# Performance work log

Hardware: AMD Instinct MI355X
Metric: run time of the kernel (lower is better)

Reference implementation:

```python
import jax, jax.numpy as jnp
import numpy as np

N_NODES = 100000
N_EDGES = 3200000
N_GRAPHS = 512
N_LAYERS = 4
D = 24  # in/out channels of every TransformerConv (mask keeps all 24 features)


def _linear_params(key, fan_in, fan_out):
    k1, k2 = jax.random.split(key)
    bound = 1.0 / np.sqrt(fan_in)
    W = jax.random.uniform(k1, (fan_in, fan_out), minval=-bound, maxval=bound, dtype=jnp.float32)
    b = jax.random.uniform(k2, (fan_out,), minval=-bound, maxval=bound, dtype=jnp.float32)
    return W, b


def setup_inputs() -> dict:
    key = jax.random.key(0)
    ks = jax.random.split(key, 32)
    x = jax.random.normal(ks[0], (N_NODES, D), dtype=jnp.float32)
    edge_index = jax.random.randint(ks[1], (2, N_EDGES), 0, N_NODES, dtype=jnp.int64)
    batch = jnp.sort(jax.random.randint(ks[2], (N_NODES,), 0, N_GRAPHS, dtype=jnp.int64))
    gf = jax.random.normal(ks[3], (N_GRAPHS, 6), dtype=jnp.float32)

    # TransformerConv params per layer: lin_query/key/value/skip, all Linear(D, D) with bias
    Wq, bq, Wk, bk, Wv, bv, Ws, bs = [], [], [], [], [], [], [], []
    for l in range(N_LAYERS):
        kk = jax.random.split(ks[4 + l], 4)
        for W_list, b_list, kw in ((Wq, bq, kk[0]), (Wk, bk, kk[1]), (Wv, bv, kk[2]), (Ws, bs, kk[3])):
            W, b = _linear_params(kw, D, D)
            W_list.append(W); b_list.append(b)
    stack = lambda xs: jnp.stack(xs, axis=0)

    gfW1, gfb1 = _linear_params(ks[10], 6, 12)
    gfW2, gfb2 = _linear_params(ks[11], 12, 12)
    W1, b1 = _linear_params(ks[12], 36, 128)
    W2, b2 = _linear_params(ks[13], 128, 128)
    W3, b3 = _linear_params(ks[14], 128, 1)

    return dict(x=x, edge_index=edge_index, batch=batch, gf=gf,
                Wq=stack(Wq), bq=stack(bq), Wk=stack(Wk), bk=stack(bk),
                Wv=stack(Wv), bv=stack(bv), Ws=stack(Ws), bs=stack(bs),
                gfW1=gfW1, gfb1=gfb1, gfW2=gfW2, gfb2=gfb2,
                W1=W1, b1=b1, W2=W2, b2=b2, W3=W3, b3=b3)


def _transformer_conv(x, src, dst, Wq, bq, Wk, bk, Wv, bv, Ws, bs):
    # PyG TransformerConv, heads=1: alpha_e = softmax_dst((q[dst].k[src])/sqrt(D));
    # out = sum_e alpha_e * v[src] (scattered to dst) + lin_skip(x)
    n = x.shape[0]
    q = x @ Wq + bq
    k = x @ Wk + bk
    v = x @ Wv + bv
    logits = jnp.sum(q[dst] * k[src], axis=-1) * (1.0 / np.sqrt(D))  # [E]
    m = jax.ops.segment_max(logits, dst, num_segments=n)  # [N]; -inf for empty dst (unused)
    e = jnp.exp(logits - m[dst])
    denom = jax.ops.segment_sum(e, dst, num_segments=n) + 1e-16
    alpha = e / denom[dst]  # [E]
    agg = jax.ops.segment_sum(alpha[:, None] * v[src], dst, num_segments=n)  # [N, D]
    return agg + (x @ Ws + bs)


def reference(x, edge_index, batch, gf, Wq, bq, Wk, bk, Wv, bv, Ws, bs,
              gfW1, gfb1, gfW2, gfb2, W1, b1, W2, b2, W3, b3):
    src, dst = edge_index[0], edge_index[1]
    h = x  # mask keeps all 24 features
    for l in range(N_LAYERS):
        h = jax.nn.relu(_transformer_conv(h, src, dst, Wq[l], bq[l], Wk[l], bk[l],
                                          Wv[l], bv[l], Ws[l], bs[l]))
    # global_mean_pool over ragged graph batch
    sums = jax.ops.segment_sum(h, batch, num_segments=N_GRAPHS)
    counts = jax.ops.segment_sum(jnp.ones((h.shape[0],), h.dtype), batch, num_segments=N_GRAPHS)
    pooled = sums / jnp.maximum(counts, 1.0)[:, None]  # [G, 24]
    g = jax.nn.relu(gf @ gfW1 + gfb1)
    g = jax.nn.relu(g @ gfW2 + gfb2)  # [G, 12]
    z = jnp.concatenate([pooled, g], axis=1)  # [G, 36]
    z = jax.nn.relu(z @ W1 + b1)
    z = jax.nn.relu(z @ W2 + b2)
    z = z @ W3 + b3
    return jnp.squeeze(z, axis=-1)  # [G]
```

## Files before the change

### kernel.cpp

```cpp
#include <hip/hip_runtime.h>
#include <hip/hip_fp16.h>
#include <math.h>

#define N_NODES  100000
#define N_EDGES  3200000
#define N_GRAPHS 512
#define DCH      24
#define NLAYERS  4

#define BINSHIFT 9
#define BINSZ    512
#define NBINS    196
#define NBINS_P  200
#define CAP      17408
#define EPB      8000
#define NB_PART  400

#define KVROW    64

__global__ __launch_bounds__(256) void lin_kernel(
    const float* __restrict__ h,
    const float* __restrict__ Wq, const float* __restrict__ bq,
    const float* __restrict__ Wk, const float* __restrict__ bk,
    const float* __restrict__ Wv, const float* __restrict__ bv,
    const float* __restrict__ Ws, const float* __restrict__ bs,
    float* __restrict__ q, __half* __restrict__ kv, float* __restrict__ skip)
{
    __shared__ float sW[4 * 576];
    __shared__ float sb[4 * 24];
    for (int i = threadIdx.x; i < 576; i += blockDim.x) {
        sW[0 * 576 + i] = Wq[i];
        sW[1 * 576 + i] = Wk[i];
        sW[2 * 576 + i] = Wv[i];
        sW[3 * 576 + i] = Ws[i];
    }
    if (threadIdx.x < 24) {
        sb[0 * 24 + threadIdx.x] = bq[threadIdx.x];
        sb[1 * 24 + threadIdx.x] = bk[threadIdx.x];
        sb[2 * 24 + threadIdx.x] = bv[threadIdx.x];
        sb[3 * 24 + threadIdx.x] = bs[threadIdx.x];
    }
    __syncthreads();

    int node = blockIdx.x * blockDim.x + threadIdx.x;
    if (node >= N_NODES) return;

    float hx[24];
    const float4* hp = (const float4*)(h + (size_t)node * DCH);
    #pragma unroll
    for (int t = 0; t < 6; t++) {
        float4 f = hp[t];
        hx[4*t] = f.x; hx[4*t+1] = f.y; hx[4*t+2] = f.z; hx[4*t+3] = f.w;
    }

    #pragma unroll
    for (int mtx = 0; mtx < 4; mtx++) {
        float o[24];
        #pragma unroll
        for (int c = 0; c < 24; c++) o[c] = sb[mtx * 24 + c];
        #pragma unroll
        for (int ci = 0; ci < 24; ci++) {
            float hv = hx[ci];
            #pragma unroll
            for (int c = 0; c < 24; c++)
                o[c] += hv * sW[mtx * 576 + ci * 24 + c];
        }
        if (mtx == 0 || mtx == 3) {
            float* dst = (mtx == 0) ? (q + (size_t)node * DCH)
                                    : (skip + (size_t)node * DCH);
            float4* op = (float4*)dst;
            #pragma unroll
            for (int t = 0; t < 6; t++) {
                float4 f;
                f.x = o[4*t]; f.y = o[4*t+1]; f.z = o[4*t+2]; f.w = o[4*t+3];
                op[t] = f;
            }
        } else {
            __half tmp[24];
            #pragma unroll
            for (int c = 0; c < 24; c++) tmp[c] = __float2half_rn(o[c]);
            float4* op = (float4*)(kv + (size_t)node * KVROW + (mtx == 1 ? 0 : 24));
            const float4* tp = (const float4*)tmp;
            #pragma unroll
            for (int t = 0; t < 3; t++) op[t] = tp[t];
        }
    }
}

__global__ void cursor_init_kernel(int* __restrict__ cursor)
{
    int t = blockIdx.x * 256 + threadIdx.x;
    if (t < NBINS) cursor[t] = t * CAP;
}

__global__ __launch_bounds__(512) void partition_kernel(
    const int* __restrict__ esrc, const int* __restrict__ edst,
    int* __restrict__ cursor, unsigned int* __restrict__ bucket)
{
    __shared__ int hist[NBINS_P];
    __shared__ int base[NBINS_P];
    for (int t = threadIdx.x; t < NBINS_P; t += 512) hist[t] = 0;
    __syncthreads();
    int e0 = blockIdx.x * EPB;
    int e1 = min(e0 + EPB, N_EDGES);
    for (int e = e0 + threadIdx.x; e < e1; e += 512)
        atomicAdd(&hist[edst[e] >> BINSHIFT], 1);
    __syncthreads();
    for (int t = threadIdx.x; t < NBINS; t += 512) {
        int hcount = hist[t];
        base[t] = hcount ? atomicAdd(&cursor[t], hcount) : 0;
    }
    __syncthreads();
    for (int t = threadIdx.x; t < NBINS_P; t += 512) hist[t] = 0;
    __syncthreads();
    for (int e = e0 + threadIdx.x; e < e1; e += 512) {
        int d = edst[e];
        int b = d >> BINSHIFT;
        int lc = atomicAdd(&hist[b], 1);
        int pos = base[b] + lc;
        if (pos < (b + 1) * CAP)
            bucket[pos] = ((unsigned)(d & (BINSZ - 1)) << 17) | (unsigned)esrc[e];
    }
}

__global__ __launch_bounds__(256) void bin_scan_kernel(
    const int* __restrict__ cursor,
    int* __restrict__ bin_base, int* __restrict__ row_start)
{
    __shared__ int sd[256];
    int t = threadIdx.x;
    int v = 0;
    if (t < NBINS) v = min(cursor[t] - t * CAP, CAP);
    sd[t] = v;
    __syncthreads();
    for (int off = 1; off < 256; off <<= 1) {
        int u = (t >= off) ? sd[t - off] : 0;
        __syncthreads();
        sd[t] += u;
        __syncthreads();
    }
    if (t < NBINS) bin_base[t] = sd[t] - v;
    if (t == 0) { bin_base[NBINS] = N_EDGES; row_start[N_NODES] = N_EDGES; }
}

__global__ __launch_bounds__(512) void bin_scatter_kernel(
    const unsigned int* __restrict__ bucket, const int* __restrict__ cursor,
    const int* __restrict__ bin_base,
    int* __restrict__ row_start, int* __restrict__ csr_src)
{
    int b = blockIdx.x;
    int node0 = b << BINSHIFT;
    int nn = min(BINSZ, N_NODES - node0);
    int ebeg = b * CAP;
    int cnt  = min(cursor[b] - b * CAP, CAP);
    int obase = bin_base[b];
    __shared__ int c0[BINSZ], s[BINSZ], cur[BINSZ];
    int tid = threadIdx.x;
    c0[tid] = 0;
    __syncthreads();
    for (int i = tid; i < cnt; i += 512)
        atomicAdd(&c0[bucket[ebeg + i] >> 17], 1);
    __syncthreads();
    s[tid] = c0[tid];
    __syncthreads();
    for (int off = 1; off < 512; off <<= 1) {
        int u = (tid >= off) ? s[tid - off] : 0;
        __syncthreads();
        s[tid] += u;
        __syncthreads();
    }
    if (tid < nn) {
        int ex = obase + s[tid] - c0[tid];
        row_start[node0 + tid] = ex;
        cur[tid] = ex;
    }
    __syncthreads();
    for (int i = tid; i < cnt; i += 512) {
        unsigned p = bucket[ebeg + i];
        int j = p >> 17;
        int pos = atomicAdd(&cur[j], 1);
        csr_src[pos] = (int)(p & 0x1FFFF);
    }
}

#define LPN 8
__global__ __launch_bounds__(256) void attn_kernel(
    const float* __restrict__ q, const __half* __restrict__ kv,
    const float* __restrict__ skip,
    const int* __restrict__ row_start,
    const int* __restrict__ csr_src,
    float* __restrict__ out)
{
    int i   = blockIdx.x * (256 / LPN) + (threadIdx.x >> 3);
    int sub = threadIdx.x & (LPN - 1);
    if (i >= N_NODES) return;

    float qr[24];
    const float4* qp = (const float4*)(q + (size_t)i * DCH);
    #pragma unroll
    for (int t = 0; t < 6; t++) {
        float4 f = qp[t];
        qr[4*t] = f.x; qr[4*t+1] = f.y; qr[4*t+2] = f.z; qr[4*t+3] = f.w;
    }

    float m = -INFINITY, s = 0.f;
    float acc[24];
    #pragma unroll
    for (int c = 0; c < 24; c++) acc[c] = 0.f;

    int beg = row_start[i];
    int end = row_start[i + 1];
    const float scale = 0.2041241452319315f;

    int src_next = (beg + sub < end) ? csr_src[beg + sub] : 0;
    for (int e = beg + sub; e < end; e += LPN) {
        int src = src_next;
        src_next = (e + LPN < end) ? csr_src[e + LPN] : 0;

        const float4* kvp = (const float4*)(kv + (size_t)src * KVROW);
        float4 kr[3], vr[3];
        #pragma unroll
        for (int t = 0; t < 3; t++) kr[t] = kvp[t];
        #pragma unroll
        for (int t = 0; t < 3; t++) vr[t] = kvp[3 + t];

        const __half2* kh = (const __half2*)kr;
        float dot = 0.f;
        #pragma unroll
        for (int j = 0; j < 12; j++) {
            float2 f = __half22float2(kh[j]);
            dot += qr[2*j] * f.x + qr[2*j+1] * f.y;
        }
        dot *= scale;

        float mn   = fmaxf(m, dot);
        float wold = __expf(m - mn);
        float w    = __expf(dot - mn);
        s = s * wold + w;
        const __half2* vh = (const __half2*)vr;
        #pragma unroll
        for (int j = 0; j < 12; j++) {
            float2 f = __half22float2(vh[j]);
            acc[2*j]   = acc[2*j]   * wold + w * f.x;
            acc[2*j+1] = acc[2*j+1] * wold + w * f.y;
        }
        m = mn;
    }

    #pragma unroll
    for (int off = 1; off < LPN; off <<= 1) {
        float m2 = __shfl_xor(m, off);
        float s2 = __shfl_xor(s, off);
        float mn = fmaxf(m, m2);
        float w1 = (m  == mn) ? 1.f : __expf(m  - mn);
        float w2 = (m2 == mn) ? 1.f : __expf(m2 - mn);
        s = s * w1 + s2 * w2;
        #pragma unroll
        for (int c = 0; c < 24; c++) {
            float a2 = __shfl_xor(acc[c], off);
            acc[c] = acc[c] * w1 + a2 * w2;
        }
        m = mn;
    }

    if (sub == 0) {
        float inv = 1.f / (s + 1e-16f);
        const float4* sp = (const float4*)(skip + (size_t)i * DCH);
        float4* op = (float4*)(out + (size_t)i * DCH);
        #pragma unroll
        for (int t = 0; t < 6; t++) {
            float4 sk = sp[t];
            float4 r;
            r.x = fmaxf(sk.x + acc[4*t]   * inv, 0.f);
            r.y = fmaxf(sk.y + acc[4*t+1] * inv, 0.f);
            r.z = fmaxf(sk.z + acc[4*t+2] * inv, 0.f);
            r.w = fmaxf(sk.w + acc[4*t+3] * inv, 0.f);
            op[t] = r;
        }
    }
}

__global__ __launch_bounds__(256) void pool_kernel(
    const float* __restrict__ h, const int* __restrict__ batch,
    float* __restrict__ pool, float* __restrict__ pcnt)
{
    __shared__ float sp[16][25];
    for (int t = threadIdx.x; t < 16 * 25; t += 256) ((float*)sp)[t] = 0.f;
    __syncthreads();

    int base = blockIdx.x * 256;
    int g0 = batch[base];
    int i = base + threadIdx.x;
    bool valid = (i < N_NODES);
    int g = valid ? batch[i] : -1;

    float hx[24];
    if (valid) {
        const float4* hp = (const float4*)(h + (size_t)i * DCH);
        #pragma unroll
        for (int t = 0; t < 6; t++) {
            float4 f = hp[t];
            hx[4*t] = f.x; hx[4*t+1] = f.y; hx[4*t+2] = f.z; hx[4*t+3] = f.w;
        }
    } else {
        #pragma unroll
        for (int c = 0; c < 24; c++) hx[c] = 0.f;
    }

    int gfirst = __shfl(g, 0);
    bool uniform = __all(valid && (g == gfirst));
    if (uniform) {
        #pragma unroll
        for (int off = 1; off < 64; off <<= 1) {
            #pragma unroll
            for (int c = 0; c < 24; c++) hx[c] += __shfl_xor(hx[c], off);
        }
        if ((threadIdx.x & 63) == 0) {
            int rel = g - g0;
            if (rel < 16) {
                #pragma unroll
                for (int c = 0; c < 24; c++) atomicAdd(&sp[rel][c], hx[c]);
                atomicAdd(&sp[rel][24], 64.f);
            } else {
                #pragma unroll
                for (int c = 0; c < 24; c++) atomicAdd(&pool[g * DCH + c], hx[c]);
                atomicAdd(&pcnt[g], 64.f);
            }
        }
    } else if (valid) {
        int rel = g - g0;
        if (rel < 16) {
            #pragma unroll
            for (int c = 0; c < 24; c++) atomicAdd(&sp[rel][c], hx[c]);
            atomicAdd(&sp[rel][24], 1.f);
        } else {
            #pragma unroll
            for (int c = 0; c < 24; c++) atomicAdd(&pool[g * DCH + c], hx[c]);
            atomicAdd(&pcnt[g], 1.f);
        }
    }
    __syncthreads();

    for (int t = threadIdx.x; t < 16 * 25; t += 256) {
        int slot = t / 25, c = t % 25;
        float val = sp[slot][c];
        if (val != 0.f) {
            int g2 = g0 + slot;
            if (c < 24) atomicAdd(&pool[g2 * DCH + c], val);
            else        atomicAdd(&pcnt[g2], val);
        }
    }
}

__global__ __launch_bounds__(128) void mlp_kernel(
    const float* __restrict__ pool, const float* __restrict__ pcnt,
    const float* __restrict__ gf,
    const float* __restrict__ gfW1, const float* __restrict__ gfb1,
    const float* __restrict__ gfW2, const float* __restrict__ gfb2,
    const float* __restrict__ W1, const float* __restrict__ b1,
    const float* __restrict__ W2, const float* __restrict__ b2,
    const float* __restrict__ W3, const float* __restrict__ b3,
    float* __restrict__ out)
{
    int g = blockIdx.x;
    int t = threadIdx.x;
    __shared__ float z[36];
    __shared__ float g1[12];
    __shared__ float h1[128];
    __shared__ float h2[128];
    __shared__ float wsum[2];

    if (t < 12) {
        float a = gfb1[t];
        #pragma unroll
        for (int j = 0; j < 6; j++) a += gf[g * 6 + j] * gfW1[j * 12 + t];
        g1[t] = fmaxf(a, 0.f);
    }
    if (t < 24) {
        float c = fmaxf(pcnt[g], 1.f);
        z[t] = pool[g * DCH + t] / c;
    }
    __syncthreads();
    if (t < 12) {
        float a = gfb2[t];
        #pragma unroll
        for (int j = 0; j < 12; j++) a += g1[j] * gfW2[j * 12 + t];
        z[24 + t] = fmaxf(a, 0.f);
    }
    __syncthreads();
    {
        float a = b1[t];
        #pragma unroll
        for (int j = 0; j < 36; j++) a += z[j] * W1[j * 128 + t];
        h1[t] = fmaxf(a, 0.f);
    }
    __syncthreads();
    {
        float a = b2[t];
        for (int j = 0; j < 128; j++) a += h1[j] * W2[j * 128 + t];
        h2[t] = fmaxf(a, 0.f);
    }
    __syncthreads();
    float p = h2[t] * W3[t];
    for (int off = 32; off; off >>= 1) p += __shfl_down(p, off);
    if ((t & 63) == 0) wsum[t >> 6] = p;
    __syncthreads();
    if (t == 0) out[g] = wsum[0] + wsum[1] + b3[0];
}

extern "C" void kernel_launch(void* const* d_in, const int* in_sizes, int n_in,
                              void* d_out, int out_size, void* d_ws, size_t ws_size,
                              hipStream_t stream)
{
    const float* x     = (const float*)d_in[0];
    const int*   ei    = (const int*)d_in[1];
    const int*   batch = (const int*)d_in[2];
    const float* gf    = (const float*)d_in[3];
    const float* Wq    = (const float*)d_in[4];
    const float* bq    = (const float*)d_in[5];
    const float* Wk    = (const float*)d_in[6];
    const float* bk    = (const float*)d_in[7];
    const float* Wv    = (const float*)d_in[8];
    const float* bv    = (const float*)d_in[9];
    const float* Ws    = (const float*)d_in[10];
    const float* bs    = (const float*)d_in[11];
    const float* gfW1  = (const float*)d_in[12];
    const float* gfb1  = (const float*)d_in[13];
    const float* gfW2  = (const float*)d_in[14];
    const float* gfb2  = (const float*)d_in[15];
    const float* W1    = (const float*)d_in[16];
    const float* b1    = (const float*)d_in[17];
    const float* W2    = (const float*)d_in[18];
    const float* b2    = (const float*)d_in[19];
    const float* W3    = (const float*)d_in[20];
    const float* b3    = (const float*)d_in[21];
    float* out = (float*)d_out;

    const int* esrc = ei;
    const int* edst = ei + N_EDGES;

    char* ws = (char*)d_ws;
    size_t off = 0;
    auto alloc = [&](size_t bytes) -> void* {
        void* p = ws + off;
        off = (off + bytes + 255) & ~(size_t)255;
        return p;
    };
    float* q     = (float*)alloc((size_t)N_NODES * DCH * 4);
    __half* kv   = (__half*)alloc((size_t)N_NODES * KVROW * 2);
    float* hA    = (float*)alloc((size_t)N_NODES * DCH * 4);
    float* hB    = (float*)alloc((size_t)N_NODES * DCH * 4);
    int* row_start   = (int*)alloc(((size_t)N_NODES + 1) * 4);
    int* csr_src     = (int*)alloc((size_t)N_EDGES * 4);
    unsigned int* bucket = (unsigned int*)alloc((size_t)NBINS * CAP * 4);
    int* bin_base    = (int*)alloc((size_t)(NBINS + 1) * 4);
    int* bin_cursor  = (int*)alloc((size_t)NBINS_P * 4);
    float* pool      = (float*)alloc((size_t)N_GRAPHS * DCH * 4);
    float* pcnt      = (float*)alloc((size_t)N_GRAPHS * 4);

    const int NB_NODE = (N_NODES + 255) / 256;
    const int NB_ATTN = (N_NODES * LPN + 255) / 256;

    cursor_init_kernel<<<1, 256, 0, stream>>>(bin_cursor);
    partition_kernel<<<NB_PART, 512, 0, stream>>>(esrc, edst, bin_cursor, bucket);
    bin_scan_kernel<<<1, 256, 0, stream>>>(bin_cursor, bin_base, row_start);
    bin_scatter_kernel<<<NBINS, 512, 0, stream>>>(bucket, bin_cursor, bin_base, row_start, csr_src);

    const float* hin = x;
    float* hbuf[2] = {hA, hB};
    for (int l = 0; l < NLAYERS; l++) {
        float* hout = hbuf[l & 1];
        lin_kernel<<<NB_NODE, 256, 0, stream>>>(
            hin, Wq + l * 576, bq + l * 24, Wk + l * 576, bk + l * 24,
            Wv + l * 576, bv + l * 24, Ws + l * 576, bs + l * 24,
            q, kv, hout);
        attn_kernel<<<NB_ATTN, 256, 0, stream>>>(
            q, kv, hout, row_start, csr_src, hout);
        hin = hout;
    }

    hipMemsetAsync(pool, 0, (size_t)N_GRAPHS * DCH * 4, stream);
    hipMemsetAsync(pcnt, 0, (size_t)N_GRAPHS * 4, stream);
    pool_kernel<<<NB_NODE, 256, 0, stream>>>(hin, batch, pool, pcnt);
    mlp_kernel<<<N_GRAPHS, 128, 0, stream>>>(
        pool, pcnt, gf, gfW1, gfb1, gfW2, gfb2, W1, b1, W2, b2, W3, b3, out);
}
```

Before: 388.1 us.

## Fuse query/skip projections and final pooling into attention kernel

The per-layer linear kernel now computes only K and V. The query and skip projections move into the attention kernel, which stages each block's 32 node rows and the Wq/Ws weights in shared memory, with each of 8 lanes computing 3 output channels. The last layer's attention kernel also does the global mean pool through shared-memory and global atomics, so the separate pool kernel and the q/skip buffers go away. This removes a global round trip for q and skip plus one launch, at the cost of extra shared-memory use and per-block weight loads in the attention kernel.

After: 406.7 us. 4.8% more time.

```diff
diff --git a/kernel.cpp b/kernel.cpp
--- a/kernel.cpp
+++ b/kernel.cpp
@@ -18,31 +18,25 @@
 
 #define KVROW    64
 
-__global__ __launch_bounds__(256) void lin_kernel(
+__global__ __launch_bounds__(256) void kv_kernel(
     const float* __restrict__ h,
-    const float* __restrict__ Wq, const float* __restrict__ bq,
     const float* __restrict__ Wk, const float* __restrict__ bk,
     const float* __restrict__ Wv, const float* __restrict__ bv,
-    const float* __restrict__ Ws, const float* __restrict__ bs,
-    float* __restrict__ q, __half* __restrict__ kv, float* __restrict__ skip)
-{
-    __shared__ float sW[4 * 576];
-    __shared__ float sb[4 * 24];
-    for (int i = threadIdx.x; i < 576; i += blockDim.x) {
-        sW[0 * 576 + i] = Wq[i];
-        sW[1 * 576 + i] = Wk[i];
-        sW[2 * 576 + i] = Wv[i];
-        sW[3 * 576 + i] = Ws[i];
+    __half* __restrict__ kv)
+{
+    __shared__ float sW[2 * 576];
+    __shared__ float sb[2 * 24];
+    for (int i = threadIdx.x; i < 576; i += 256) {
+        sW[i] = Wk[i];
+        sW[576 + i] = Wv[i];
     }
     if (threadIdx.x < 24) {
-        sb[0 * 24 + threadIdx.x] = bq[threadIdx.x];
-        sb[1 * 24 + threadIdx.x] = bk[threadIdx.x];
-        sb[2 * 24 + threadIdx.x] = bv[threadIdx.x];
-        sb[3 * 24 + threadIdx.x] = bs[threadIdx.x];
-    }
-    __syncthreads();
-
-    int node = blockIdx.x * blockDim.x + threadIdx.x;
+        sb[threadIdx.x] = bk[threadIdx.x];
+        sb[24 + threadIdx.x] = bv[threadIdx.x];
+    }
+    __syncthreads();
+
+    int node = blockIdx.x * 256 + threadIdx.x;
     if (node >= N_NODES) return;
 
     float hx[24];
@@ -54,7 +48,7 @@
     }
 
     #pragma unroll
-    for (int mtx = 0; mtx < 4; mtx++) {
+    for (int mtx = 0; mtx < 2; mtx++) {
         float o[24];
         #pragma unroll
         for (int c = 0; c < 24; c++) o[c] = sb[mtx * 24 + c];
@@ -65,25 +59,13 @@
             for (int c = 0; c < 24; c++)
                 o[c] += hv * sW[mtx * 576 + ci * 24 + c];
         }
-        if (mtx == 0 || mtx == 3) {
-            float* dst = (mtx == 0) ? (q + (size_t)node * DCH)
-                                    : (skip + (size_t)node * DCH);
-            float4* op = (float4*)dst;
-            #pragma unroll
-            for (int t = 0; t < 6; t++) {
-                float4 f;
-                f.x = o[4*t]; f.y = o[4*t+1]; f.z = o[4*t+2]; f.w = o[4*t+3];
-                op[t] = f;
-            }
-        } else {
-            __half tmp[24];
-            #pragma unroll
-            for (int c = 0; c < 24; c++) tmp[c] = __float2half_rn(o[c]);
-            float4* op = (float4*)(kv + (size_t)node * KVROW + (mtx == 1 ? 0 : 24));
-            const float4* tp = (const float4*)tmp;
-            #pragma unroll
-            for (int t = 0; t < 3; t++) op[t] = tp[t];
-        }
+        __half tmp[24];
+        #pragma unroll
+        for (int c = 0; c < 24; c++) tmp[c] = __float2half_rn(o[c]);
+        float4* op = (float4*)(kv + (size_t)node * KVROW + mtx * 24);
+        const float4* tp = (const float4*)tmp;
+        #pragma unroll
+        for (int t = 0; t < 3; t++) op[t] = tp[t];
     }
 }
 
@@ -183,25 +165,55 @@
     }
 }
 
-#define LPN 8
+template<int DO_POOL>
 __global__ __launch_bounds__(256) void attn_kernel(
-    const float* __restrict__ q, const __half* __restrict__ kv,
-    const float* __restrict__ skip,
-    const int* __restrict__ row_start,
-    const int* __restrict__ csr_src,
-    float* __restrict__ out)
-{
-    int i   = blockIdx.x * (256 / LPN) + (threadIdx.x >> 3);
-    int sub = threadIdx.x & (LPN - 1);
-    if (i >= N_NODES) return;
+    const float* __restrict__ h, const __half* __restrict__ kv,
+    const float* __restrict__ Wq, const float* __restrict__ bq,
+    const float* __restrict__ Ws, const float* __restrict__ bs,
+    const int* __restrict__ row_start, const int* __restrict__ csr_src,
+    const int* __restrict__ batch,
+    float* __restrict__ out, float* __restrict__ poolc)
+{
+    __shared__ float sWq[576], sWs[576];
+    __shared__ float sbq[24], sbs[24];
+    __shared__ float sh[32 * 24];
+    __shared__ float sq[32 * 24];
+    __shared__ float spool[8][25];
+
+    int tid = threadIdx.x;
+    for (int t = tid; t < 576; t += 256) { sWq[t] = Wq[t]; sWs[t] = Ws[t]; }
+    if (tid < 24) { sbq[tid] = bq[tid]; sbs[tid] = bs[tid]; }
+    if (DO_POOL) {
+        for (int t = tid; t < 8 * 25; t += 256) ((float*)spool)[t] = 0.f;
+    }
+    int node0 = blockIdx.x * 32;
+    for (int t = tid; t < 192; t += 256)
+        ((float4*)sh)[t] = ((const float4*)(h + (size_t)node0 * DCH))[t];
+    __syncthreads();
+
+    int grp = tid >> 3;
+    int sub = tid & 7;
+    int i = node0 + grp;
+
+    {
+        const float* hrow = &sh[grp * 24];
+        float qc0 = sbq[3*sub], qc1 = sbq[3*sub+1], qc2 = sbq[3*sub+2];
+        #pragma unroll
+        for (int ci = 0; ci < 24; ci++) {
+            float hv = hrow[ci];
+            qc0 += hv * sWq[ci*24 + 3*sub];
+            qc1 += hv * sWq[ci*24 + 3*sub + 1];
+            qc2 += hv * sWq[ci*24 + 3*sub + 2];
+        }
+        sq[grp*24 + 3*sub]     = qc0;
+        sq[grp*24 + 3*sub + 1] = qc1;
+        sq[grp*24 + 3*sub + 2] = qc2;
+    }
+    __syncthreads();
 
     float qr[24];
-    const float4* qp = (const float4*)(q + (size_t)i * DCH);
     #pragma unroll
-    for (int t = 0; t < 6; t++) {
-        float4 f = qp[t];
-        qr[4*t] = f.x; qr[4*t+1] = f.y; qr[4*t+2] = f.z; qr[4*t+3] = f.w;
-    }
+    for (int c = 0; c < 24; c++) qr[c] = sq[grp*24 + c];
 
     float m = -INFINITY, s = 0.f;
     float acc[24];
@@ -213,9 +225,9 @@
     const float scale = 0.2041241452319315f;
 
     int src_next = (beg + sub < end) ? csr_src[beg + sub] : 0;
-    for (int e = beg + sub; e < end; e += LPN) {
+    for (int e = beg + sub; e < end; e += 8) {
         int src = src_next;
-        src_next = (e + LPN < end) ? csr_src[e + LPN] : 0;
+        src_next = (e + 8 < end) ? csr_src[e + 8] : 0;
 
         const float4* kvp = (const float4*)(kv + (size_t)src * KVROW);
         float4 kr[3], vr[3];
@@ -248,7 +260,7 @@
     }
 
     #pragma unroll
-    for (int off = 1; off < LPN; off <<= 1) {
+    for (int off = 1; off < 8; off <<= 1) {
         float m2 = __shfl_xor(m, off);
         float s2 = __shfl_xor(s, off);
         float mn = fmaxf(m, m2);
@@ -263,97 +275,53 @@
         m = mn;
     }
 
-    if (sub == 0) {
+    float o0, o1, o2;
+    {
+        const float* hrow = &sh[grp * 24];
+        float k0 = sbs[3*sub], k1 = sbs[3*sub+1], k2 = sbs[3*sub+2];
+        #pragma unroll
+        for (int ci = 0; ci < 24; ci++) {
+            float hv = hrow[ci];
+            k0 += hv * sWs[ci*24 + 3*sub];
+            k1 += hv * sWs[ci*24 + 3*sub + 1];
+            k2 += hv * sWs[ci*24 + 3*sub + 2];
+        }
         float inv = 1.f / (s + 1e-16f);
-        const float4* sp = (const float4*)(skip + (size_t)i * DCH);
-        float4* op = (float4*)(out + (size_t)i * DCH);
-        #pragma unroll
-        for (int t = 0; t < 6; t++) {
-            float4 sk = sp[t];
-            float4 r;
-            r.x = fmaxf(sk.x + acc[4*t]   * inv, 0.f);
-            r.y = fmaxf(sk.y + acc[4*t+1] * inv, 0.f);
-            r.z = fmaxf(sk.z + acc[4*t+2] * inv, 0.f);
-            r.w = fmaxf(sk.w + acc[4*t+3] * inv, 0.f);
-            op[t] = r;
-        }
-    }
-}
-
-__global__ __launch_bounds__(256) void pool_kernel(
-    const float* __restrict__ h, const int* __restrict__ batch,
-    float* __restrict__ pool, float* __restrict__ pcnt)
-{
-    __shared__ float sp[16][25];
-    for (int t = threadIdx.x; t < 16 * 25; t += 256) ((float*)sp)[t] = 0.f;
-    __syncthreads();
-
-    int base = blockIdx.x * 256;
-    int g0 = batch[base];
-    int i = base + threadIdx.x;
-    bool valid = (i < N_NODES);
-    int g = valid ? batch[i] : -1;
-
-    float hx[24];
-    if (valid) {
-        const float4* hp = (const float4*)(h + (size_t)i * DCH);
-        #pragma unroll
-        for (int t = 0; t < 6; t++) {
-            float4 f = hp[t];
-            hx[4*t] = f.x; hx[4*t+1] = f.y; hx[4*t+2] = f.z; hx[4*t+3] = f.w;
-        }
+        o0 = fmaxf(k0 + acc[3*sub]     * inv, 0.f);
+        o1 = fmaxf(k1 + acc[3*sub + 1] * inv, 0.f);
+        o2 = fmaxf(k2 + acc[3*sub + 2] * inv, 0.f);
+    }
+
+    if (!DO_POOL) {
+        size_t base = (size_t)i * DCH + 3*sub;
+        out[base] = o0; out[base + 1] = o1; out[base + 2] = o2;
     } else {
-        #pragma unroll
-        for (int c = 0; c < 24; c++) hx[c] = 0.f;
-    }
-
-    int gfirst = __shfl(g, 0);
-    bool uniform = __all(valid && (g == gfirst));
-    if (uniform) {
-        #pragma unroll
-        for (int off = 1; off < 64; off <<= 1) {
-            #pragma unroll
-            for (int c = 0; c < 24; c++) hx[c] += __shfl_xor(hx[c], off);
-        }
-        if ((threadIdx.x & 63) == 0) {
-            int rel = g - g0;
-            if (rel < 16) {
-                #pragma unroll
-                for (int c = 0; c < 24; c++) atomicAdd(&sp[rel][c], hx[c]);
-                atomicAdd(&sp[rel][24], 64.f);
-            } else {
-                #pragma unroll
-                for (int c = 0; c < 24; c++) atomicAdd(&pool[g * DCH + c], hx[c]);
-                atomicAdd(&pcnt[g], 64.f);
-            }
-        }
-    } else if (valid) {
+        int g  = batch[i];
+        int g0 = batch[node0];
         int rel = g - g0;
-        if (rel < 16) {
-            #pragma unroll
-            for (int c = 0; c < 24; c++) atomicAdd(&sp[rel][c], hx[c]);
-            atomicAdd(&sp[rel][24], 1.f);
+        if (rel < 8) {
+            atomicAdd(&spool[rel][3*sub],     o0);
+            atomicAdd(&spool[rel][3*sub + 1], o1);
+            atomicAdd(&spool[rel][3*sub + 2], o2);
+            if (sub == 0) atomicAdd(&spool[rel][24], 1.f);
         } else {
-            #pragma unroll
-            for (int c = 0; c < 24; c++) atomicAdd(&pool[g * DCH + c], hx[c]);
-            atomicAdd(&pcnt[g], 1.f);
-        }
-    }
-    __syncthreads();
-
-    for (int t = threadIdx.x; t < 16 * 25; t += 256) {
-        int slot = t / 25, c = t % 25;
-        float val = sp[slot][c];
-        if (val != 0.f) {
-            int g2 = g0 + slot;
-            if (c < 24) atomicAdd(&pool[g2 * DCH + c], val);
-            else        atomicAdd(&pcnt[g2], val);
+            atomicAdd(&poolc[g * 25 + 3*sub],     o0);
+            atomicAdd(&poolc[g * 25 + 3*sub + 1], o1);
+            atomicAdd(&poolc[g * 25 + 3*sub + 2], o2);
+            if (sub == 0) atomicAdd(&poolc[g * 25 + 24], 1.f);
+        }
+        __syncthreads();
+        for (int t = tid; t < 8 * 25; t += 256) {
+            int slot = t / 25, c = t % 25;
+            float val = spool[slot][c];
+            if (val != 0.f)
+                atomicAdd(&poolc[(g0 + slot) * 25 + c], val);
         }
     }
 }
 
 __global__ __launch_bounds__(128) void mlp_kernel(
-    const float* __restrict__ pool, const float* __restrict__ pcnt,
+    const float* __restrict__ poolc,
     const float* __restrict__ gf,
     const float* __restrict__ gfW1, const float* __restrict__ gfb1,
     const float* __restrict__ gfW2, const float* __restrict__ gfb2,
@@ -377,8 +345,8 @@
         g1[t] = fmaxf(a, 0.f);
     }
     if (t < 24) {
-        float c = fmaxf(pcnt[g], 1.f);
-        z[t] = pool[g * DCH + t] / c;
+        float c = fmaxf(poolc[g * 25 + 24], 1.f);
+        z[t] = poolc[g * 25 + t] / c;
     }
     __syncthreads();
     if (t < 12) {
@@ -446,7 +414,6 @@
         off = (off + bytes + 255) & ~(size_t)255;
         return p;
     };
-    float* q     = (float*)alloc((size_t)N_NODES * DCH * 4);
     __half* kv   = (__half*)alloc((size_t)N_NODES * KVROW * 2);
     float* hA    = (float*)alloc((size_t)N_NODES * DCH * 4);
     float* hB    = (float*)alloc((size_t)N_NODES * DCH * 4);
@@ -455,33 +422,36 @@
     unsigned int* bucket = (unsigned int*)alloc((size_t)NBINS * CAP * 4);
     int* bin_base    = (int*)alloc((size_t)(NBINS + 1) * 4);
     int* bin_cursor  = (int*)alloc((size_t)NBINS_P * 4);
-    float* pool      = (float*)alloc((size_t)N_GRAPHS * DCH * 4);
-    float* pcnt      = (float*)alloc((size_t)N_GRAPHS * 4);
+    float* poolc     = (float*)alloc((size_t)N_GRAPHS * 25 * 4);
 
     const int NB_NODE = (N_NODES + 255) / 256;
-    const int NB_ATTN = (N_NODES * LPN + 255) / 256;
+    const int NB_ATTN = N_NODES / 32;
 
     cursor_init_kernel<<<1, 256, 0, stream>>>(bin_cursor);
     partition_kernel<<<NB_PART, 512, 0, stream>>>(esrc, edst, bin_cursor, bucket);
     bin_scan_kernel<<<1, 256, 0, stream>>>(bin_cursor, bin_base, row_start);
     bin_scatter_kernel<<<NBINS, 512, 0, stream>>>(bucket, bin_cursor, bin_base, row_start, csr_src);
 
+    hipMemsetAsync(poolc, 0, (size_t)N_GRAPHS * 25 * 4, stream);
+
     const float* hin = x;
     float* hbuf[2] = {hA, hB};
     for (int l = 0; l < NLAYERS; l++) {
-        float* hout = hbuf[l & 1];
-        lin_kernel<<<NB_NODE, 256, 0, stream>>>(
-            hin, Wq + l * 576, bq + l * 24, Wk + l * 576, bk + l * 24,
-            Wv + l * 576, bv + l * 24, Ws + l * 576, bs + l * 24,
-            q, kv, hout);
-        attn_kernel<<<NB_ATTN, 256, 0, stream>>>(
-            q, kv, hout, row_start, csr_src, hout);
-        hin = hout;
-    }
-
-    hipMemsetAsync(pool, 0, (size_t)N_GRAPHS * DCH * 4, stream);
-    hipMemsetAsync(pcnt, 0, (size_t)N_GRAPHS * 4, stream);
-    pool_kernel<<<NB_NODE, 256, 0, stream>>>(hin, batch, pool, pcnt);
+        kv_kernel<<<NB_NODE, 256, 0, stream>>>(
+            hin, Wk + l * 576, bk + l * 24, Wv + l * 576, bv + l * 24, kv);
+        if (l < NLAYERS - 1) {
+            float* hout = hbuf[l & 1];
+            attn_kernel<0><<<NB_ATTN, 256, 0, stream>>>(
+                hin, kv, Wq + l * 576, bq + l * 24, Ws + l * 576, bs + l * 24,
+                row_start, csr_src, batch, hout, nullptr);
+            hin = hout;
+        } else {
+            attn_kernel<1><<<NB_ATTN, 256, 0, stream>>>(
+                hin, kv, Wq + l * 576, bq + l * 24, Ws + l * 576, bs + l * 24,
+                row_start, csr_src, batch, nullptr, poolc);
+        }
+    }
+
     mlp_kernel<<<N_GRAPHS, 128, 0, stream>>>(
-        pool, pcnt, gf, gfW1, gfb1, gfW2, gfb2, W1, b1, W2, b2, W3, b3, out);
-}
+        poolc, gf, gfW1, gfb1, gfW2, gfb2, W1, b1, W2, b2, W3, b3, out);
+}
```

## Fuse global mean pooling into final attention layer kernel

Applied to the files above, without the earlier changes.

The last attention layer is templated to accumulate per-graph sums and counts directly into a combined pool/count buffer through shared-memory atomics, with fallback to global atomics. This removes the separate pool kernel, its re-read of the final hidden state, the final-layer output write, and one memset. The skip output now always goes to a dedicated buffer. In exchange, the last attention kernel takes on extra shared atomics and a block-wide sync, and the early-return-before-sync pattern only stays safe because the node count divides the block size exactly.

Result: faster. 377.6 us (-2.7%).

```diff
diff --git a/kernel.cpp b/kernel.cpp
--- a/kernel.cpp
+++ b/kernel.cpp
@@ -184,14 +184,23 @@
 }
 
 #define LPN 8
+template<int DO_POOL>
 __global__ __launch_bounds__(256) void attn_kernel(
     const float* __restrict__ q, const __half* __restrict__ kv,
     const float* __restrict__ skip,
     const int* __restrict__ row_start,
     const int* __restrict__ csr_src,
-    float* __restrict__ out)
-{
-    int i   = blockIdx.x * (256 / LPN) + (threadIdx.x >> 3);
+    const int* __restrict__ batch,
+    float* __restrict__ out, float* __restrict__ poolc)
+{
+    __shared__ float spool[8][25];
+    int node0 = blockIdx.x * (256 / LPN);
+    if (DO_POOL) {
+        for (int t = threadIdx.x; t < 8 * 25; t += 256) ((float*)spool)[t] = 0.f;
+        __syncthreads();
+    }
+
+    int i   = node0 + (threadIdx.x >> 3);
     int sub = threadIdx.x & (LPN - 1);
     if (i >= N_NODES) return;
 
@@ -263,97 +272,55 @@
         m = mn;
     }
 
-    if (sub == 0) {
+    if (!DO_POOL) {
+        if (sub == 0) {
+            float inv = 1.f / (s + 1e-16f);
+            const float4* sp = (const float4*)(skip + (size_t)i * DCH);
+            float4* op = (float4*)(out + (size_t)i * DCH);
+            #pragma unroll
+            for (int t = 0; t < 6; t++) {
+                float4 sk = sp[t];
+                float4 r;
+                r.x = fmaxf(sk.x + acc[4*t]   * inv, 0.f);
+                r.y = fmaxf(sk.y + acc[4*t+1] * inv, 0.f);
+                r.z = fmaxf(sk.z + acc[4*t+2] * inv, 0.f);
+                r.w = fmaxf(sk.w + acc[4*t+3] * inv, 0.f);
+                op[t] = r;
+            }
+        }
+    } else {
         float inv = 1.f / (s + 1e-16f);
-        const float4* sp = (const float4*)(skip + (size_t)i * DCH);
-        float4* op = (float4*)(out + (size_t)i * DCH);
-        #pragma unroll
-        for (int t = 0; t < 6; t++) {
-            float4 sk = sp[t];
-            float4 r;
-            r.x = fmaxf(sk.x + acc[4*t]   * inv, 0.f);
-            r.y = fmaxf(sk.y + acc[4*t+1] * inv, 0.f);
-            r.z = fmaxf(sk.z + acc[4*t+2] * inv, 0.f);
-            r.w = fmaxf(sk.w + acc[4*t+3] * inv, 0.f);
-            op[t] = r;
-        }
-    }
-}
-
-__global__ __launch_bounds__(256) void pool_kernel(
-    const float* __restrict__ h, const int* __restrict__ batch,
-    float* __restrict__ pool, float* __restrict__ pcnt)
-{
-    __shared__ float sp[16][25];
-    for (int t = threadIdx.x; t < 16 * 25; t += 256) ((float*)sp)[t] = 0.f;
-    __syncthreads();
-
-    int base = blockIdx.x * 256;
-    int g0 = batch[base];
-    int i = base + threadIdx.x;
-    bool valid = (i < N_NODES);
-    int g = valid ? batch[i] : -1;
-
-    float hx[24];
-    if (valid) {
-        const float4* hp = (const float4*)(h + (size_t)i * DCH);
-        #pragma unroll
-        for (int t = 0; t < 6; t++) {
-            float4 f = hp[t];
-            hx[4*t] = f.x; hx[4*t+1] = f.y; hx[4*t+2] = f.z; hx[4*t+3] = f.w;
-        }
-    } else {
-        #pragma unroll
-        for (int c = 0; c < 24; c++) hx[c] = 0.f;
-    }
-
-    int gfirst = __shfl(g, 0);
-    bool uniform = __all(valid && (g == gfirst));
-    if (uniform) {
-        #pragma unroll
-        for (int off = 1; off < 64; off <<= 1) {
-            #pragma unroll
-            for (int c = 0; c < 24; c++) hx[c] += __shfl_xor(hx[c], off);
-        }
-        if ((threadIdx.x & 63) == 0) {
-            int rel = g - g0;
-            if (rel < 16) {
-                #pragma unroll
-                for (int c = 0; c < 24; c++) atomicAdd(&sp[rel][c], hx[c]);
-                atomicAdd(&sp[rel][24], 64.f);
-            } else {
-                #pragma unroll
-                for (int c = 0; c < 24; c++) atomicAdd(&pool[g * DCH + c], hx[c]);
-                atomicAdd(&pcnt[g], 64.f);
-            }
-        }
-    } else if (valid) {
+        const float* sp = skip + (size_t)i * DCH + 3 * sub;
+        float o0 = fmaxf(sp[0] + acc[3*sub]     * inv, 0.f);
+        float o1 = fmaxf(sp[1] + acc[3*sub + 1] * inv, 0.f);
+        float o2 = fmaxf(sp[2] + acc[3*sub + 2] * inv, 0.f);
+        int g  = batch[i];
+        int g0 = batch[node0];
         int rel = g - g0;
-        if (rel < 16) {
-            #pragma unroll
-            for (int c = 0; c < 24; c++) atomicAdd(&sp[rel][c], hx[c]);
-            atomicAdd(&sp[rel][24], 1.f);
+        if (rel < 8) {
+            atomicAdd(&spool[rel][3*sub],     o0);
+            atomicAdd(&spool[rel][3*sub + 1], o1);
+            atomicAdd(&spool[rel][3*sub + 2], o2);
+            if (sub == 0) atomicAdd(&spool[rel][24], 1.f);
         } else {
-            #pragma unroll
-            for (int c = 0; c < 24; c++) atomicAdd(&pool[g * DCH + c], hx[c]);
-            atomicAdd(&pcnt[g], 1.f);
-        }
-    }
-    __syncthreads();
-
-    for (int t = threadIdx.x; t < 16 * 25; t += 256) {
-        int slot = t / 25, c = t % 25;
-        float val = sp[slot][c];
-        if (val != 0.f) {
-            int g2 = g0 + slot;
-            if (c < 24) atomicAdd(&pool[g2 * DCH + c], val);
-            else        atomicAdd(&pcnt[g2], val);
+            atomicAdd(&poolc[g * 25 + 3*sub],     o0);
+            atomicAdd(&poolc[g * 25 + 3*sub + 1], o1);
+            atomicAdd(&poolc[g * 25 + 3*sub + 2], o2);
+            if (sub == 0) atomicAdd(&poolc[g * 25 + 24], 1.f);
+        }
+        __syncthreads();
+        int g0b = batch[node0];
+        for (int t = threadIdx.x; t < 8 * 25; t += 256) {
+            int slot = t / 25, c = t % 25;
+            float val = spool[slot][c];
+            if (val != 0.f)
+                atomicAdd(&poolc[(g0b + slot) * 25 + c], val);
         }
     }
 }
 
 __global__ __launch_bounds__(128) void mlp_kernel(
-    const float* __restrict__ pool, const float* __restrict__ pcnt,
+    const float* __restrict__ poolc,
     const float* __restrict__ gf,
     const float* __restrict__ gfW1, const float* __restrict__ gfb1,
     const float* __restrict__ gfW2, const float* __restrict__ gfb2,
@@ -377,8 +344,8 @@
         g1[t] = fmaxf(a, 0.f);
     }
     if (t < 24) {
-        float c = fmaxf(pcnt[g], 1.f);
-        z[t] = pool[g * DCH + t] / c;
+        float c = fmaxf(poolc[g * 25 + 24], 1.f);
+        z[t] = poolc[g * 25 + t] / c;
     }
     __syncthreads();
     if (t < 12) {
@@ -450,13 +417,13 @@
     __half* kv   = (__half*)alloc((size_t)N_NODES * KVROW * 2);
     float* hA    = (float*)alloc((size_t)N_NODES * DCH * 4);
     float* hB    = (float*)alloc((size_t)N_NODES * DCH * 4);
+    float* skipb = (float*)alloc((size_t)N_NODES * DCH * 4);
     int* row_start   = (int*)alloc(((size_t)N_NODES + 1) * 4);
     int* csr_src     = (int*)alloc((size_t)N_EDGES * 4);
     unsigned int* bucket = (unsigned int*)alloc((size_t)NBINS * CAP * 4);
     int* bin_base    = (int*)alloc((size_t)(NBINS + 1) * 4);
     int* bin_cursor  = (int*)alloc((size_t)NBINS_P * 4);
-    float* pool      = (float*)alloc((size_t)N_GRAPHS * DCH * 4);
-    float* pcnt      = (float*)alloc((size_t)N_GRAPHS * 4);
+    float* poolc     = (float*)alloc((size_t)N_GRAPHS * 25 * 4);
 
     const int NB_NODE = (N_NODES + 255) / 256;
     const int NB_ATTN = (N_NODES * LPN + 255) / 256;
@@ -466,22 +433,27 @@
     bin_scan_kernel<<<1, 256, 0, stream>>>(bin_cursor, bin_base, row_start);
     bin_scatter_kernel<<<NBINS, 512, 0, stream>>>(bucket, bin_cursor, bin_base, row_start, csr_src);
 
+    hipMemsetAsync(poolc, 0, (size_t)N_GRAPHS * 25 * 4, stream);
+
     const float* hin = x;
     float* hbuf[2] = {hA, hB};
     for (int l = 0; l < NLAYERS; l++) {
-        float* hout = hbuf[l & 1];
+        float* hout = (l < NLAYERS - 1) ? hbuf[l & 1] : nullptr;
+        float* sk   = (l < NLAYERS - 1) ? hout : skipb;
         lin_kernel<<<NB_NODE, 256, 0, stream>>>(
             hin, Wq + l * 576, bq + l * 24, Wk + l * 576, bk + l * 24,
             Wv + l * 576, bv + l * 24, Ws + l * 576, bs + l * 24,
-            q, kv, hout);
-        attn_kernel<<<NB_ATTN, 256, 0, stream>>>(
-            q, kv, hout, row_start, csr_src, hout);
-        hin = hout;
-    }
-
-    hipMemsetAsync(pool, 0, (size_t)N_GRAPHS * DCH * 4, stream);
-    hipMemsetAsync(pcnt, 0, (size_t)N_GRAPHS * 4, stream);
-    pool_kernel<<<NB_NODE, 256, 0, stream>>>(hin, batch, pool, pcnt);
+            q, kv, skipb);
+        if (l < NLAYERS - 1) {
+            attn_kernel<0><<<NB_ATTN, 256, 0, stream>>>(
+                q, kv, skipb, row_start, csr_src, batch, hout, nullptr);
+            hin = hout;
+        } else {
+            attn_kernel<1><<<NB_ATTN, 256, 0, stream>>>(
+                q, kv, skipb, row_start, csr_src, batch, nullptr, poolc);
+        }
+    }
+
     mlp_kernel<<<N_GRAPHS, 128, 0, stream>>>(
-        pool, pcnt, gf, gfW1, gfb1, gfW2, gfb2, W1, b1, W2, b2, W3, b3, out);
-}
+        poolc, gf, gfW1, gfb1, gfW2, gfb2, W1, b1, W2, b2, W3, b3, out);
+}
```
